# Optimization experiments

Measured on AMD Instinct MI355X. Metric: run time of the kernel, lower is better.

Reference implementation:

```python
import jax, jax.numpy as jnp
import numpy as np
from jax import lax

MARGIN = 0.3
BIGF = 1e9


def _pairwise_dist(x):
    # dist[i,j] = ||x_i - x_j||, clamped at 1e-12 before sqrt (as in torch code)
    sq = jnp.sum(x * x, axis=1)
    d = sq[:, None] + sq[None, :] - 2.0 * (x @ x.T)
    return jnp.sqrt(jnp.clip(d, 1e-12))


def _hard_mining(dist, targets):
    is_pos = targets[:, None] == targets[None, :]
    ap = jnp.where(is_pos, dist, jnp.asarray(-BIGF, dist.dtype))
    an = jnp.where(is_pos, jnp.asarray(BIGF, dist.dtype), dist)
    dist_ap = jnp.max(ap, axis=1)
    p_inds = jnp.argmax(ap, axis=1)
    dist_an = jnp.min(an, axis=1)
    n_inds = jnp.argmin(an, axis=1)
    return dist_ap, dist_an, p_inds, n_inds


def _batch_euclidean(x, y):
    # x: [N,m,d], y: [N,n,d] -> [N,m,n]
    xx = jnp.sum(x * x, axis=-1)[:, :, None]
    yy = jnp.sum(y * y, axis=-1)[:, None, :]
    d = xx + yy - 2.0 * jnp.einsum('nmd,nkd->nmk', x, y)
    return jnp.sqrt(jnp.clip(d, 1e-12))


def _shortest_dist(dmat):
    # DTW-style shortest path over [m,n] grid, batched over N: dp[i,j] = d[i,j] + min(dp[i-1,j], dp[i,j-1])
    N, m, n = dmat.shape
    big = jnp.asarray(BIGF, dmat.dtype)
    init_row = jnp.full((N, n), big, dmat.dtype).at[:, 0].set(0.0)  # virtual row -1: only (0,0) reachable

    def row_step(prev_row, drow):  # prev_row,drow: [N,n]
        def col_step(left, un):  # left: [N]
            up, d = un
            cur = d + jnp.minimum(up, left)
            return cur, cur
        _, cols = lax.scan(col_step, jnp.full((N,), big, dmat.dtype), (prev_row.T, drow.T))
        return cols.T, None

    last_row, _ = lax.scan(row_step, init_row, jnp.moveaxis(dmat, 1, 0))
    return last_row[:, -1]


def _batch_local_dist(x, y):
    d = _batch_euclidean(x, y)
    d = jnp.tanh(d * 0.5)  # == (exp(d)-1)/(exp(d)+1), numerically safe
    return _shortest_dist(d)


def _margin_ranking(dist_an, dist_ap, margin):
    # MarginRankingLoss with y=1: mean(relu(margin - (dist_an - dist_ap)))
    return jnp.mean(jnp.maximum(0.0, margin + dist_ap - dist_an))


def setup_inputs() -> dict:
    key = jax.random.key(0)
    k1, k2 = jax.random.split(key)
    N, D = 512, 2048
    LD, PARTS = 128, 8
    K = 4  # instances per identity (PK sampling)
    inputs = jax.random.normal(k1, (N, D), dtype=jnp.float32)
    local_features = jax.random.normal(k2, (N, LD, PARTS), dtype=jnp.float32)
    targets = jnp.arange(N, dtype=jnp.int64) // K
    return {"inputs": inputs, "targets": targets, "local_features": local_features}


def reference(inputs, targets, local_features):
    dist = _pairwise_dist(inputs)
    dist_ap, dist_an, p_inds, n_inds = _hard_mining(dist, targets)
    global_loss = _margin_ranking(dist_an, dist_ap, MARGIN)
    lf = jnp.transpose(local_features, (0, 2, 1))  # [N, parts, local_dim]
    local_ap = _batch_local_dist(lf, lf[p_inds])
    local_an = _batch_local_dist(lf, lf[n_inds])
    local_loss = _margin_ranking(local_an, local_ap, MARGIN)
    return (global_loss, local_loss)
```

## Files before the change

kernel.cpp:

```cpp
#include <hip/hip_runtime.h>
#include <math.h>

#define MARGIN 0.3f
#define BIGF 1e9f
#define NN 512
#define DD 2048
#define LDIM 128
#define PARTS 8

typedef __attribute__((ext_vector_type(8))) __bf16 bf16x8;
typedef __attribute__((ext_vector_type(4))) __bf16 bf16x4;
typedef __attribute__((ext_vector_type(4))) float f32x4;

__device__ __forceinline__ void load_lds16(const void* g, void* lds) {
    __builtin_amdgcn_global_load_lds(
        (const __attribute__((address_space(1))) unsigned int*)g,
        (__attribute__((address_space(3))) unsigned int*)lds, 16, 0, 0);
}

__global__ __launch_bounds__(256) void k_prep(
    const float* __restrict__ X, __bf16* __restrict__ Hhi, __bf16* __restrict__ Hlo,
    float* __restrict__ norms, float* gsum, float* lsum, unsigned* counter)
{
    int i = blockIdx.x;
    int t = threadIdx.x;
    const float4* xr = (const float4*)(X + (size_t)i * DD);
    float4 v1 = xr[t];
    float4 v2 = xr[t + 256];
    float acc = v1.x * v1.x + v1.y * v1.y + v1.z * v1.z + v1.w * v1.w
              + v2.x * v2.x + v2.y * v2.y + v2.z * v2.z + v2.w * v2.w;

    float e1[4] = {v1.x, v1.y, v1.z, v1.w};
    float e2[4] = {v2.x, v2.y, v2.z, v2.w};
    bf16x4 h1, h2, l1, l2;
#pragma unroll
    for (int j = 0; j < 4; j++) {
        __bf16 h = (__bf16)e1[j];
        h1[j] = h;
        l1[j] = (__bf16)(e1[j] - (float)h);
        __bf16 g = (__bf16)e2[j];
        h2[j] = g;
        l2[j] = (__bf16)(e2[j] - (float)g);
    }
    bf16x4* hr = (bf16x4*)(Hhi + (size_t)i * DD);
    bf16x4* lr = (bf16x4*)(Hlo + (size_t)i * DD);
    hr[t] = h1; hr[t + 256] = h2;
    lr[t] = l1; lr[t + 256] = l2;

    for (int off = 32; off > 0; off >>= 1)
        acc += __shfl_down(acc, off);
    __shared__ float part[4];
    int lane = t & 63, wid = t >> 6;
    if (lane == 0) part[wid] = acc;
    __syncthreads();
    if (t == 0) {
        norms[i] = part[0] + part[1] + part[2] + part[3];
        if (i == 0) { *gsum = 0.0f; *lsum = 0.0f; *counter = 0u; }
    }
}

__global__ __launch_bounds__(256) void k_gram_mfma(
    const __bf16* __restrict__ Hhi, const __bf16* __restrict__ Hlo,
    float* __restrict__ Gp)
{
    __shared__ __bf16 Ah[2048], Al[2048], Bh[2048], Bl[2048];

    int bid = blockIdx.x;
    int tj = bid & 7;
    int ti = (bid >> 3) & 7;
    int ks = bid >> 6;
    int t = threadIdx.x;
    int w = t >> 6, lane = t & 63;
    int wr = w >> 1, wc = w & 1;

    int row16 = (w << 4) + (lane & 15);
    int kchunk = (lane >> 4) << 3;
    size_t kc0 = (size_t)(ks * 512 + kchunk);
    const __bf16* pAh = Hhi + (size_t)(ti * 64 + row16) * DD + kc0;
    const __bf16* pAl = Hlo + (size_t)(ti * 64 + row16) * DD + kc0;
    const __bf16* pBh = Hhi + (size_t)(tj * 64 + row16) * DD + kc0;
    const __bf16* pBl = Hlo + (size_t)(tj * 64 + row16) * DD + kc0;
    __bf16* ldsAh = &Ah[w * 512];
    __bf16* ldsAl = &Al[w * 512];
    __bf16* ldsBh = &Bh[w * 512];
    __bf16* ldsBl = &Bl[w * 512];

    f32x4 acc00 = {0.f, 0.f, 0.f, 0.f};
    f32x4 acc01 = {0.f, 0.f, 0.f, 0.f};
    f32x4 acc10 = {0.f, 0.f, 0.f, 0.f};
    f32x4 acc11 = {0.f, 0.f, 0.f, 0.f};

    for (int it = 0; it < 16; ++it) {
        load_lds16(pAh, ldsAh);
        load_lds16(pBh, ldsBh);
        load_lds16(pAl, ldsAl);
        load_lds16(pBl, ldsBl);
        pAh += 32; pAl += 32; pBh += 32; pBl += 32;
        __syncthreads();

        const bf16x8* fAh = (const bf16x8*)&Ah[wr * 1024];
        const bf16x8* fAl = (const bf16x8*)&Al[wr * 1024];
        const bf16x8* fBh = (const bf16x8*)&Bh[wc * 1024];
        const bf16x8* fBl = (const bf16x8*)&Bl[wc * 1024];
        bf16x8 ah0 = fAh[lane], ah1 = fAh[lane + 64];
        bf16x8 al0 = fAl[lane], al1 = fAl[lane + 64];
        bf16x8 bh0 = fBh[lane], bh1 = fBh[lane + 64];
        bf16x8 bl0 = fBl[lane], bl1 = fBl[lane + 64];

        acc00 = __builtin_amdgcn_mfma_f32_16x16x32_bf16(ah0, bh0, acc00, 0, 0, 0);
        acc00 = __builtin_amdgcn_mfma_f32_16x16x32_bf16(ah0, bl0, acc00, 0, 0, 0);
        acc00 = __builtin_amdgcn_mfma_f32_16x16x32_bf16(al0, bh0, acc00, 0, 0, 0);

        acc01 = __builtin_amdgcn_mfma_f32_16x16x32_bf16(ah0, bh1, acc01, 0, 0, 0);
        acc01 = __builtin_amdgcn_mfma_f32_16x16x32_bf16(ah0, bl1, acc01, 0, 0, 0);
        acc01 = __builtin_amdgcn_mfma_f32_16x16x32_bf16(al0, bh1, acc01, 0, 0, 0);

        acc10 = __builtin_amdgcn_mfma_f32_16x16x32_bf16(ah1, bh0, acc10, 0, 0, 0);
        acc10 = __builtin_amdgcn_mfma_f32_16x16x32_bf16(ah1, bl0, acc10, 0, 0, 0);
        acc10 = __builtin_amdgcn_mfma_f32_16x16x32_bf16(al1, bh0, acc10, 0, 0, 0);

        acc11 = __builtin_amdgcn_mfma_f32_16x16x32_bf16(ah1, bh1, acc11, 0, 0, 0);
        acc11 = __builtin_amdgcn_mfma_f32_16x16x32_bf16(ah1, bl1, acc11, 0, 0, 0);
        acc11 = __builtin_amdgcn_mfma_f32_16x16x32_bf16(al1, bh1, acc11, 0, 0, 0);
        __syncthreads();
    }

    int rbase = ti * 64 + wr * 32 + ((lane >> 4) << 2);
    int cbase = tj * 64 + wc * 32 + (lane & 15);
    float* gb = Gp + (size_t)ks * NN * NN;
    f32x4 accs[2][2] = {{acc00, acc01}, {acc10, acc11}};
#pragma unroll
    for (int g = 0; g < 2; g++)
#pragma unroll
        for (int h = 0; h < 2; h++)
#pragma unroll
            for (int r = 0; r < 4; r++)
                gb[(size_t)(rbase + g * 16 + r) * NN + cbase + h * 16] = accs[g][h][r];
}

__global__ __launch_bounds__(256) void k_mine_local(
    const float* __restrict__ Gp, const float* __restrict__ norms,
    const int* __restrict__ tg, const float* __restrict__ LF,
    float* gsum, float* lsum, unsigned* counter, float* __restrict__ out)
{
    __shared__ float s_apv[4]; __shared__ int s_api[4];
    __shared__ float s_anv[4]; __shared__ int s_ani[4];
    __shared__ int sh_pn[2];
    __shared__ float A[LDIM * PARTS];
    __shared__ float B[2][LDIM * PARTS];
    __shared__ float dtm[2][64];
    __shared__ float res[2];

    int i = blockIdx.x;
    int t = threadIdx.x;
    float ni = norms[i];
    int tgt_i = tg[i];

    float apv = -BIGF; int api = 0x7fffffff;
    float anv =  BIGF; int ani = 0x7fffffff;

#pragma unroll
    for (int jj = 0; jj < 2; jj++) {
        int j = t + jj * 256;
        size_t base = (size_t)i * NN + j;
        float g = Gp[base] + Gp[base + (size_t)NN * NN]
                + Gp[base + 2ul * NN * NN] + Gp[base + 3ul * NN * NN];
        float dd = ni + norms[j] - 2.0f * g;
        float dist = sqrtf(fmaxf(dd, 1e-12f));
        bool pos = (tg[j] == tgt_i);
        float a = pos ? dist : -BIGF;
        if (a > apv || (a == apv && j < api)) { apv = a; api = j; }
        float b = pos ? BIGF : dist;
        if (b < anv || (b == anv && j < ani)) { anv = b; ani = j; }
    }
    for (int off = 32; off > 0; off >>= 1) {
        float av = __shfl_down(apv, off); int ai = __shfl_down(api, off);
        if (av > apv || (av == apv && ai < api)) { apv = av; api = ai; }
        float nv = __shfl_down(anv, off); int nid = __shfl_down(ani, off);
        if (nv < anv || (nv == anv && nid < ani)) { anv = nv; ani = nid; }
    }
    int lane = t & 63, wid = t >> 6;
    if (lane == 0) { s_apv[wid] = apv; s_api[wid] = api;
                     s_anv[wid] = anv; s_ani[wid] = ani; }
    __syncthreads();
    if (t == 0) {
        apv = s_apv[0]; api = s_api[0]; anv = s_anv[0]; ani = s_ani[0];
        for (int wv = 1; wv < 4; wv++) {
            float av = s_apv[wv]; int ai = s_api[wv];
            if (av > apv || (av == apv && ai < api)) { apv = av; api = ai; }
            float nv = s_anv[wv]; int nid = s_ani[wv];
            if (nv < anv || (nv == anv && nid < ani)) { anv = nv; ani = nid; }
        }
        sh_pn[0] = api;
        sh_pn[1] = ani;
        atomicAdd(gsum, fmaxf(0.0f, MARGIN + apv - anv));
    }
    __syncthreads();

    int w = t >> 6;
    ((float4*)A)[t] = ((const float4*)(LF + (size_t)i * LDIM * PARTS))[t];
    if (w < 2) {
        int ind = sh_pn[w];
        const float4* B4 = (const float4*)(LF + (size_t)ind * LDIM * PARTS);
        float4* Bw = (float4*)B[w];
        Bw[lane]       = B4[lane];
        Bw[lane + 64]  = B4[lane + 64];
        Bw[lane + 128] = B4[lane + 128];
        Bw[lane + 192] = B4[lane + 192];
    }
    __syncthreads();

    if (w < 2) {
        int p = lane >> 3, q = lane & 7;
        float acc = 0.0f;
        const float* Bw = B[w];
        for (int d = 0; d < LDIM; d++) {
            float diff = A[d * PARTS + p] - Bw[d * PARTS + q];
            acc = fmaf(diff, diff, acc);
        }
        float dist = sqrtf(fmaxf(acc, 1e-12f));
        dtm[w][p * 8 + q] = tanhf(0.5f * dist);
    }
    __syncthreads();

    if ((t == 0) || (t == 64)) {
        const float* dm = dtm[w];
        float dp[8];
        dp[0] = dm[0];
        for (int j = 1; j < 8; j++) dp[j] = dp[j - 1] + dm[j];
        for (int r = 1; r < 8; r++) {
            dp[0] += dm[r * 8];
            for (int j = 1; j < 8; j++)
                dp[j] = dm[r * 8 + j] + fminf(dp[j], dp[j - 1]);
        }
        res[w] = dp[7];
    }
    __syncthreads();

    if (t == 0) {
        float l = fmaxf(0.0f, MARGIN + res[0] - res[1]);
        atomicAdd(lsum, l);
        __threadfence();
        unsigned old = atomicAdd(counter, 1u);
        if (old == (NN - 1)) {
            __threadfence();
            float ls = atomicAdd(lsum, 0.0f);
            float gs = atomicAdd(gsum, 0.0f);
            out[0] = gs * (1.0f / NN);
            out[1] = ls * (1.0f / NN);
        }
    }
}

extern "C" void kernel_launch(void* const* d_in, const int* in_sizes, int n_in,
                              void* d_out, int out_size, void* d_ws, size_t ws_size,
                              hipStream_t stream)
{
    const float* X  = (const float*)d_in[0];
    const int*   tg = (const int*)d_in[1];
    const float* LF = (const float*)d_in[2];
    float* out = (float*)d_out;

    char* ws = (char*)d_ws;
    float*    Gp      = (float*)ws;
    __bf16*   Hhi     = (__bf16*)(ws + (4u << 20));
    __bf16*   Hlo     = (__bf16*)(ws + (6u << 20));
    float*    norms   = (float*)(ws + (8u << 20));
    float*    gsum    = (float*)(ws + (8u << 20) + 4096);
    float*    lsum    = (float*)(ws + (8u << 20) + 4100);
    unsigned* counter = (unsigned*)(ws + (8u << 20) + 4104);

    k_prep<<<NN, 256, 0, stream>>>(X, Hhi, Hlo, norms, gsum, lsum, counter);
    k_gram_mfma<<<256, 256, 0, stream>>>(Hhi, Hlo, Gp);
    k_mine_local<<<NN, 256, 0, stream>>>(Gp, norms, tg, LF, gsum, lsum, counter, out);
}
```

Before: 100.3 us.

## Fuse bf16 split conversion into Gram kernel and derive norms from diagonal

Removes the separate prep kernel: the Gram kernel now loads fp32 rows directly, splits them into hi/lo bf16 in registers, and writes them to LDS, prefetching the next chunk during compute. Squared norms come from the diagonal tiles of the Gram accumulators rather than a separate reduction. The K split doubles to 8, giving 512 blocks, and the mining kernel sums 8 partial Gram slices. This drops one launch and the global round trip of the bf16 copies, in exchange for more partial-sum traffic and conversion work in the GEMM.

```diff
diff --git a/kernel.cpp b/kernel.cpp
--- a/kernel.cpp
+++ b/kernel.cpp
@@ -9,120 +9,95 @@
 #define PARTS 8
 
 typedef __attribute__((ext_vector_type(8))) __bf16 bf16x8;
-typedef __attribute__((ext_vector_type(4))) __bf16 bf16x4;
 typedef __attribute__((ext_vector_type(4))) float f32x4;
 
-__device__ __forceinline__ void load_lds16(const void* g, void* lds) {
-    __builtin_amdgcn_global_load_lds(
-        (const __attribute__((address_space(1))) unsigned int*)g,
-        (__attribute__((address_space(3))) unsigned int*)lds, 16, 0, 0);
-}
-
-__global__ __launch_bounds__(256) void k_prep(
-    const float* __restrict__ X, __bf16* __restrict__ Hhi, __bf16* __restrict__ Hlo,
-    float* __restrict__ norms, float* gsum, float* lsum, unsigned* counter)
+__device__ __forceinline__ void cvt8(const float4 a, const float4 b,
+                                     bf16x8& h, bf16x8& l) {
+    float f[8] = {a.x, a.y, a.z, a.w, b.x, b.y, b.z, b.w};
+#pragma unroll
+    for (int e = 0; e < 8; e++) {
+        __bf16 hh = (__bf16)f[e];
+        h[e] = hh;
+        l[e] = (__bf16)(f[e] - (float)hh);
+    }
+}
+
+__global__ __launch_bounds__(256, 2) void k_gram(
+    const float* __restrict__ X, float* __restrict__ Gp,
+    float* __restrict__ ndiag, float* gsum, float* lsum, unsigned* counter)
 {
-    int i = blockIdx.x;
-    int t = threadIdx.x;
-    const float4* xr = (const float4*)(X + (size_t)i * DD);
-    float4 v1 = xr[t];
-    float4 v2 = xr[t + 256];
-    float acc = v1.x * v1.x + v1.y * v1.y + v1.z * v1.z + v1.w * v1.w
-              + v2.x * v2.x + v2.y * v2.y + v2.z * v2.z + v2.w * v2.w;
-
-    float e1[4] = {v1.x, v1.y, v1.z, v1.w};
-    float e2[4] = {v2.x, v2.y, v2.z, v2.w};
-    bf16x4 h1, h2, l1, l2;
-#pragma unroll
-    for (int j = 0; j < 4; j++) {
-        __bf16 h = (__bf16)e1[j];
-        h1[j] = h;
-        l1[j] = (__bf16)(e1[j] - (float)h);
-        __bf16 g = (__bf16)e2[j];
-        h2[j] = g;
-        l2[j] = (__bf16)(e2[j] - (float)g);
-    }
-    bf16x4* hr = (bf16x4*)(Hhi + (size_t)i * DD);
-    bf16x4* lr = (bf16x4*)(Hlo + (size_t)i * DD);
-    hr[t] = h1; hr[t + 256] = h2;
-    lr[t] = l1; lr[t + 256] = l2;
-
-    for (int off = 32; off > 0; off >>= 1)
-        acc += __shfl_down(acc, off);
-    __shared__ float part[4];
-    int lane = t & 63, wid = t >> 6;
-    if (lane == 0) part[wid] = acc;
-    __syncthreads();
-    if (t == 0) {
-        norms[i] = part[0] + part[1] + part[2] + part[3];
-        if (i == 0) { *gsum = 0.0f; *lsum = 0.0f; *counter = 0u; }
-    }
-}
-
-__global__ __launch_bounds__(256) void k_gram_mfma(
-    const __bf16* __restrict__ Hhi, const __bf16* __restrict__ Hlo,
-    float* __restrict__ Gp)
-{
-    __shared__ __bf16 Ah[2048], Al[2048], Bh[2048], Bl[2048];
+    __shared__ __bf16 Ah[4096], Al[4096], Bh[4096], Bl[4096];
 
     int bid = blockIdx.x;
-    int tj = bid & 7;
-    int ti = (bid >> 3) & 7;
-    int ks = bid >> 6;
+    int tj = bid & 7, ti = (bid >> 3) & 7, ks = bid >> 6;
     int t = threadIdx.x;
     int w = t >> 6, lane = t & 63;
     int wr = w >> 1, wc = w & 1;
 
-    int row16 = (w << 4) + (lane & 15);
-    int kchunk = (lane >> 4) << 3;
-    size_t kc0 = (size_t)(ks * 512 + kchunk);
-    const __bf16* pAh = Hhi + (size_t)(ti * 64 + row16) * DD + kc0;
-    const __bf16* pAl = Hlo + (size_t)(ti * 64 + row16) * DD + kc0;
-    const __bf16* pBh = Hhi + (size_t)(tj * 64 + row16) * DD + kc0;
-    const __bf16* pBl = Hlo + (size_t)(tj * 64 + row16) * DD + kc0;
-    __bf16* ldsAh = &Ah[w * 512];
-    __bf16* ldsAl = &Al[w * 512];
-    __bf16* ldsBh = &Bh[w * 512];
-    __bf16* ldsBl = &Bl[w * 512];
+    if (bid == 0 && t == 0) { *gsum = 0.0f; *lsum = 0.0f; *counter = 0u; }
+
+    int m = t >> 7;
+    int r = (t >> 1) & 63;
+    int kst = t & 1;
+    int grow = (m ? tj : ti) * 64 + r;
+    const float4* gp4 = (const float4*)(X + (size_t)grow * DD + ks * 256 + kst * 32);
+    int ebase = kst * 2048 + (r >> 4) * 512 + (r & 15) * 8;
+    __bf16* hb = (m ? Bh : Ah) + ebase;
+    __bf16* lb = (m ? Bl : Al) + ebase;
+
+    float4 cur[8];
+#pragma unroll
+    for (int q = 0; q < 8; q++) cur[q] = gp4[q];
 
     f32x4 acc00 = {0.f, 0.f, 0.f, 0.f};
     f32x4 acc01 = {0.f, 0.f, 0.f, 0.f};
     f32x4 acc10 = {0.f, 0.f, 0.f, 0.f};
     f32x4 acc11 = {0.f, 0.f, 0.f, 0.f};
 
-    for (int it = 0; it < 16; ++it) {
-        load_lds16(pAh, ldsAh);
-        load_lds16(pBh, ldsBh);
-        load_lds16(pAl, ldsAl);
-        load_lds16(pBl, ldsBl);
-        pAh += 32; pAl += 32; pBh += 32; pBl += 32;
+#pragma unroll
+    for (int it = 0; it < 4; ++it) {
+        if (it > 0) __syncthreads();
+#pragma unroll
+        for (int jg = 0; jg < 4; jg++) {
+            bf16x8 h, l;
+            cvt8(cur[2 * jg], cur[2 * jg + 1], h, l);
+            *(bf16x8*)(hb + jg * 128) = h;
+            *(bf16x8*)(lb + jg * 128) = l;
+        }
+        if (it < 3) {
+            const float4* np = gp4 + (it + 1) * 16;
+#pragma unroll
+            for (int q = 0; q < 8; q++) cur[q] = np[q];
+        }
         __syncthreads();
 
-        const bf16x8* fAh = (const bf16x8*)&Ah[wr * 1024];
-        const bf16x8* fAl = (const bf16x8*)&Al[wr * 1024];
-        const bf16x8* fBh = (const bf16x8*)&Bh[wc * 1024];
-        const bf16x8* fBl = (const bf16x8*)&Bl[wc * 1024];
-        bf16x8 ah0 = fAh[lane], ah1 = fAh[lane + 64];
-        bf16x8 al0 = fAl[lane], al1 = fAl[lane + 64];
-        bf16x8 bh0 = fBh[lane], bh1 = fBh[lane + 64];
-        bf16x8 bl0 = fBl[lane], bl1 = fBl[lane + 64];
-
-        acc00 = __builtin_amdgcn_mfma_f32_16x16x32_bf16(ah0, bh0, acc00, 0, 0, 0);
-        acc00 = __builtin_amdgcn_mfma_f32_16x16x32_bf16(ah0, bl0, acc00, 0, 0, 0);
-        acc00 = __builtin_amdgcn_mfma_f32_16x16x32_bf16(al0, bh0, acc00, 0, 0, 0);
-
-        acc01 = __builtin_amdgcn_mfma_f32_16x16x32_bf16(ah0, bh1, acc01, 0, 0, 0);
-        acc01 = __builtin_amdgcn_mfma_f32_16x16x32_bf16(ah0, bl1, acc01, 0, 0, 0);
-        acc01 = __builtin_amdgcn_mfma_f32_16x16x32_bf16(al0, bh1, acc01, 0, 0, 0);
-
-        acc10 = __builtin_amdgcn_mfma_f32_16x16x32_bf16(ah1, bh0, acc10, 0, 0, 0);
-        acc10 = __builtin_amdgcn_mfma_f32_16x16x32_bf16(ah1, bl0, acc10, 0, 0, 0);
-        acc10 = __builtin_amdgcn_mfma_f32_16x16x32_bf16(al1, bh0, acc10, 0, 0, 0);
-
-        acc11 = __builtin_amdgcn_mfma_f32_16x16x32_bf16(ah1, bh1, acc11, 0, 0, 0);
-        acc11 = __builtin_amdgcn_mfma_f32_16x16x32_bf16(ah1, bl1, acc11, 0, 0, 0);
-        acc11 = __builtin_amdgcn_mfma_f32_16x16x32_bf16(al1, bh1, acc11, 0, 0, 0);
-        __syncthreads();
+#pragma unroll
+        for (int kstep = 0; kstep < 2; kstep++) {
+            const bf16x8* fAh = (const bf16x8*)&Ah[kstep * 2048 + wr * 1024];
+            const bf16x8* fAl = (const bf16x8*)&Al[kstep * 2048 + wr * 1024];
+            const bf16x8* fBh = (const bf16x8*)&Bh[kstep * 2048 + wc * 1024];
+            const bf16x8* fBl = (const bf16x8*)&Bl[kstep * 2048 + wc * 1024];
+            bf16x8 ah0 = fAh[lane], ah1 = fAh[lane + 64];
+            bf16x8 al0 = fAl[lane], al1 = fAl[lane + 64];
+            bf16x8 bh0 = fBh[lane], bh1 = fBh[lane + 64];
+            bf16x8 bl0 = fBl[lane], bl1 = fBl[lane + 64];
+
+            acc00 = __builtin_amdgcn_mfma_f32_16x16x32_bf16(ah0, bh0, acc00, 0, 0, 0);
+            acc00 = __builtin_amdgcn_mfma_f32_16x16x32_bf16(ah0, bl0, acc00, 0, 0, 0);
+            acc00 = __builtin_amdgcn_mfma_f32_16x16x32_bf16(al0, bh0, acc00, 0, 0, 0);
+
+            acc01 = __builtin_amdgcn_mfma_f32_16x16x32_bf16(ah0, bh1, acc01, 0, 0, 0);
+            acc01 = __builtin_amdgcn_mfma_f32_16x16x32_bf16(ah0, bl1, acc01, 0, 0, 0);
+            acc01 = __builtin_amdgcn_mfma_f32_16x16x32_bf16(al0, bh1, acc01, 0, 0, 0);
+
+            acc10 = __builtin_amdgcn_mfma_f32_16x16x32_bf16(ah1, bh0, acc10, 0, 0, 0);
+            acc10 = __builtin_amdgcn_mfma_f32_16x16x32_bf16(ah1, bl0, acc10, 0, 0, 0);
+            acc10 = __builtin_amdgcn_mfma_f32_16x16x32_bf16(al1, bh0, acc10, 0, 0, 0);
+
+            acc11 = __builtin_amdgcn_mfma_f32_16x16x32_bf16(ah1, bh1, acc11, 0, 0, 0);
+            acc11 = __builtin_amdgcn_mfma_f32_16x16x32_bf16(ah1, bl1, acc11, 0, 0, 0);
+            acc11 = __builtin_amdgcn_mfma_f32_16x16x32_bf16(al1, bh1, acc11, 0, 0, 0);
+        }
     }
 
     int rbase = ti * 64 + wr * 32 + ((lane >> 4) << 2);
@@ -134,15 +109,23 @@
 #pragma unroll
         for (int h = 0; h < 2; h++)
 #pragma unroll
-            for (int r = 0; r < 4; r++)
-                gb[(size_t)(rbase + g * 16 + r) * NN + cbase + h * 16] = accs[g][h][r];
+            for (int rr = 0; rr < 4; rr++)
+                gb[(size_t)(rbase + g * 16 + rr) * NN + cbase + h * 16] = accs[g][h][rr];
+
+    if (ti == tj && wr == wc && ((lane >> 4) == ((lane & 15) >> 2))) {
+        int rr = lane & 3;
+        int row0 = rbase + rr;
+        ndiag[ks * NN + row0]      = acc00[rr];
+        ndiag[ks * NN + row0 + 16] = acc11[rr];
+    }
 }
 
 __global__ __launch_bounds__(256) void k_mine_local(
-    const float* __restrict__ Gp, const float* __restrict__ norms,
+    const float* __restrict__ Gp, const float* __restrict__ ndiag,
     const int* __restrict__ tg, const float* __restrict__ LF,
     float* gsum, float* lsum, unsigned* counter, float* __restrict__ out)
 {
+    __shared__ float sdiag[NN];
     __shared__ float s_apv[4]; __shared__ int s_api[4];
     __shared__ float s_anv[4]; __shared__ int s_ani[4];
     __shared__ int sh_pn[2];
@@ -153,7 +136,18 @@
 
     int i = blockIdx.x;
     int t = threadIdx.x;
-    float ni = norms[i];
+
+    float d0 = 0.f, d1 = 0.f;
+#pragma unroll
+    for (int ks = 0; ks < 8; ks++) {
+        d0 += ndiag[ks * NN + t];
+        d1 += ndiag[ks * NN + t + 256];
+    }
+    sdiag[t] = d0;
+    sdiag[t + 256] = d1;
+    __syncthreads();
+
+    float ni = sdiag[i];
     int tgt_i = tg[i];
 
     float apv = -BIGF; int api = 0x7fffffff;
@@ -162,10 +156,12 @@
 #pragma unroll
     for (int jj = 0; jj < 2; jj++) {
         int j = t + jj * 256;
-        size_t base = (size_t)i * NN + j;
-        float g = Gp[base] + Gp[base + (size_t)NN * NN]
-                + Gp[base + 2ul * NN * NN] + Gp[base + 3ul * NN * NN];
-        float dd = ni + norms[j] - 2.0f * g;
+        float g = 0.f;
+#pragma unroll
+        for (int ks = 0; ks < 8; ks++)
+            g += Gp[(size_t)ks * NN * NN + (size_t)i * NN + j];
+        float nj = (jj == 0) ? d0 : d1;
+        float dd = ni + nj - 2.0f * g;
         float dist = sqrtf(fmaxf(dd, 1e-12f));
         bool pos = (tg[j] == tgt_i);
         float a = pos ? dist : -BIGF;
@@ -228,10 +224,10 @@
         float dp[8];
         dp[0] = dm[0];
         for (int j = 1; j < 8; j++) dp[j] = dp[j - 1] + dm[j];
-        for (int r = 1; r < 8; r++) {
-            dp[0] += dm[r * 8];
+        for (int rr = 1; rr < 8; rr++) {
+            dp[0] += dm[rr * 8];
             for (int j = 1; j < 8; j++)
-                dp[j] = dm[r * 8 + j] + fminf(dp[j], dp[j - 1]);
+                dp[j] = dm[rr * 8 + j] + fminf(dp[j], dp[j - 1]);
         }
         res[w] = dp[7];
     }
@@ -263,14 +259,11 @@
 
     char* ws = (char*)d_ws;
     float*    Gp      = (float*)ws;
-    __bf16*   Hhi     = (__bf16*)(ws + (4u << 20));
-    __bf16*   Hlo     = (__bf16*)(ws + (6u << 20));
-    float*    norms   = (float*)(ws + (8u << 20));
-    float*    gsum    = (float*)(ws + (8u << 20) + 4096);
-    float*    lsum    = (float*)(ws + (8u << 20) + 4100);
-    unsigned* counter = (unsigned*)(ws + (8u << 20) + 4104);
-
-    k_prep<<<NN, 256, 0, stream>>>(X, Hhi, Hlo, norms, gsum, lsum, counter);
-    k_gram_mfma<<<256, 256, 0, stream>>>(Hhi, Hlo, Gp);
-    k_mine_local<<<NN, 256, 0, stream>>>(Gp, norms, tg, LF, gsum, lsum, counter, out);
-}
+    float*    ndiag   = (float*)(ws + (8u << 20));
+    float*    gsum    = (float*)(ws + (8u << 20) + 16384);
+    float*    lsum    = (float*)(ws + (8u << 20) + 16388);
+    unsigned* counter = (unsigned*)(ws + (8u << 20) + 16392);
+
+    k_gram<<<512, 256, 0, stream>>>(X, Gp, ndiag, gsum, lsum, counter);
+    k_mine_local<<<512, 256, 0, stream>>>(Gp, ndiag, tg, LF, gsum, lsum, counter, out);
+}
```

Result: faster. 96.93 us (-3.4%).
